# Performance work log

Hardware: AMD Instinct MI355X
Metric: run time of the kernel (lower is better)

Reference implementation:

```python
import jax, jax.numpy as jnp
import numpy as np

N_NODES = 100000
N_EDGES = 1600000
N_GRAPHS = 512
NODE_DIM = 64   # len(node_indices)
GRAPH_DIM = 16  # len(graph_indices) == graph_channels
HIDDEN = 128
OUT = 8


def setup_inputs() -> dict:
    key = jax.random.key(0)
    ks = jax.random.split(key, 12)
    x = jax.random.normal(ks[0], (N_NODES, NODE_DIM + GRAPH_DIM), dtype=jnp.float32)
    edge_index = jax.random.randint(ks[1], (2, N_EDGES), 0, N_NODES, dtype=jnp.int64)
    batch = jnp.sort(jax.random.randint(ks[2], (N_NODES,), 0, N_GRAPHS, dtype=jnp.int64))
    def lin(k, fan_in, fan_out):
        lim = 1.0 / np.sqrt(fan_in)
        return jax.random.uniform(k, (fan_in, fan_out), jnp.float32, -lim, lim)
    return {
        "x": x, "edge_index": edge_index, "batch": batch,
        "W1": lin(ks[3], NODE_DIM, HIDDEN), "b1": jnp.zeros((HIDDEN,), jnp.float32),
        "W2": lin(ks[4], HIDDEN, HIDDEN),   "b2": jnp.zeros((HIDDEN,), jnp.float32),
        "Wm1": lin(ks[5], HIDDEN + GRAPH_DIM, HIDDEN), "bm1": jnp.zeros((HIDDEN,), jnp.float32),
        "Wm2": lin(ks[6], HIDDEN, OUT), "bm2": jnp.zeros((OUT,), jnp.float32),
    }


def _gcn_conv(h_in, src, dst, W, b):
    # PyG GCNConv: h = X W; out = D^{-1/2}(A+I)D^{-1/2} h + b, deg over A+I.
    h = h_in @ W                                        # [N, H]
    deg = jnp.zeros((N_NODES,), h.dtype).at[dst].add(1.0) + 1.0  # +1 self loop
    dinv = jax.lax.rsqrt(deg)                           # [N]
    norm = dinv[src] * dinv[dst]                        # [E]
    out = jnp.zeros_like(h).at[dst].add(norm[:, None] * h[src])
    out = out + (dinv * dinv)[:, None] * h              # self-loop term
    return out + b


def _mean_pool(v, batch):
    cnt = jax.ops.segment_sum(jnp.ones((v.shape[0],), v.dtype), batch, num_segments=N_GRAPHS)
    s = jax.ops.segment_sum(v, batch, num_segments=N_GRAPHS)
    return s / jnp.maximum(cnt, 1.0)[:, None]


def reference(x, edge_index, batch, W1, b1, W2, b2, Wm1, bm1, Wm2, bm2):
    src, dst = edge_index[0], edge_index[1]
    node_t = x[:, :NODE_DIM]                 # node_indices slice
    graph_t = _mean_pool(x[:, NODE_DIM:], batch)  # graph_indices slice, pooled [G, 16]
    h = _gcn_conv(node_t, src, dst, W1, b1)
    h = jax.nn.relu(h)                       # dropout is identity in eval mode
    h = _gcn_conv(h, src, dst, W2, b2)
    g = _mean_pool(h, batch)                 # [G, H]
    g = jnp.concatenate([g, graph_t], axis=1)
    g = jax.nn.relu(g @ Wm1 + bm1)
    return g @ Wm2 + bm2                     # [G, OUT]
```

## Files before the change

### kernel.cpp

```cpp
#include <hip/hip_runtime.h>
#include <hip/hip_bf16.h>

#define N_NODES 100000
#define N_EDGES 1600000
#define N_GRAPHS 512
#define NODE_DIM 64
#define GRAPH_DIM 16
#define HIDDEN 128
#define OUT_DIM 8

#define NBUCKETS 391
#define BIN_CAP 8192
#define EPB 4096

__device__ __forceinline__ float bflo(unsigned u) { return __uint_as_float(u << 16); }
__device__ __forceinline__ float bfhi(unsigned u) { return __uint_as_float(u & 0xffff0000u); }


__global__ __launch_bounds__(256) void k_binplace(const int* __restrict__ src,
                                                  const int* __restrict__ dst,
                                                  int* __restrict__ gcur,
                                                  unsigned* __restrict__ bin) {
    __shared__ int cnt[NBUCKETS];
    __shared__ int base[NBUCKETS];
    int t = threadIdx.x;
    for (int i = t; i < NBUCKETS; i += 256) cnt[i] = 0;
    __syncthreads();
    int e0 = blockIdx.x * EPB;
#pragma unroll
    for (int k = 0; k < EPB / 256; k++) {
        int e = e0 + k * 256 + t;
        if (e < N_EDGES) atomicAdd(&cnt[dst[e] >> 8], 1);
    }
    __syncthreads();
    for (int i = t; i < NBUCKETS; i += 256) {
        int c = cnt[i];
        base[i] = (c > 0) ? atomicAdd(&gcur[i], c) : 0;
        cnt[i] = 0;
    }
    __syncthreads();
#pragma unroll
    for (int k = 0; k < EPB / 256; k++) {
        int e = e0 + k * 256 + t;
        if (e < N_EDGES) {
            int d = dst[e];
            int b = d >> 8;
            int p = atomicAdd(&cnt[b], 1);
            bin[(size_t)b * BIN_CAP + base[b] + p] = ((unsigned)src[e] << 8) | (unsigned)(d & 255);
        }
    }
}


__global__ __launch_bounds__(256) void k_build(const int* __restrict__ gcur,
                                               const unsigned* __restrict__ bin,
                                               float* __restrict__ dinv,
                                               int2* __restrict__ rowse,
                                               int* __restrict__ csr,
                                               float* __restrict__ gt_sum) {
    __shared__ int cnt[256];
    __shared__ int sc[256];
    __shared__ int rsl[256];
    int b = blockIdx.x, t = threadIdx.x;
    if (b < 32) gt_sum[b * 256 + t] = 0.0f;
    cnt[t] = 0;
    __syncthreads();
    int n = gcur[b];
    const unsigned* seg = bin + (size_t)b * BIN_CAP;
    for (int i = t; i < n; i += 256) atomicAdd(&cnt[seg[i] & 255u], 1);
    __syncthreads();
    int deg = cnt[t];
    sc[t] = deg;
    __syncthreads();
    for (int o = 1; o < 256; o <<= 1) {
        int u = (t >= o) ? sc[t - o] : 0;
        __syncthreads();
        sc[t] += u;
        __syncthreads();
    }
    int rs = b * BIN_CAP + sc[t] - deg;
    int node = b * 256 + t;
    if (node < N_NODES) {
        dinv[node] = rsqrtf((float)deg + 1.0f);
        rowse[node] = make_int2(rs, rs + deg);
    }
    rsl[t] = rs;
    cnt[t] = 0;
    __syncthreads();
    for (int i = t; i < n; i += 256) {
        unsigned e = seg[i];
        int dlidx = (int)(e & 255u);
        csr[rsl[dlidx] + atomicAdd(&cnt[dlidx], 1)] = (int)(e >> 8);
    }
}


__global__ __launch_bounds__(256) void k_packstat(const float* __restrict__ x,
                                                  const int* __restrict__ batch,
                                                  ushort* __restrict__ xb,
                                                  float* __restrict__ gt_sum) {
    int t = threadIdx.x;
    int i0 = blockIdx.x * 64;
    for (int idx = t; idx < 64 * 32; idx += 256) {
        int node = i0 + (idx >> 5);
        if (node < N_NODES) {
            int c2 = idx & 31;
            float2 v = *(const float2*)&x[(size_t)node * 80 + c2 * 2];
            __hip_bfloat16 lo = __float2bfloat16(v.x);
            __hip_bfloat16 hi = __float2bfloat16(v.y);
            ushort2 pv = make_ushort2(*(ushort*)&lo, *(ushort*)&hi);
            ((ushort2*)xb)[(size_t)node * 32 + c2] = pv;
        }
    }
    int c = t & 15, sub = t >> 4;
    int iend = min(i0 + 64, N_NODES);
    float acc = 0.0f;
    int g = -1;
    for (int i = i0 + sub; i < iend; i += 16) {
        int bi = batch[i];
        if (bi != g) {
            if (g >= 0) atomicAdd(&gt_sum[g * GRAPH_DIM + c], acc);
            acc = 0.0f; g = bi;
        }
        acc += x[(size_t)i * 80 + NODE_DIM + c];
    }
    if (g >= 0) atomicAdd(&gt_sum[g * GRAPH_DIM + c], acc);
}


#define LDX(s_) __uint_as_float((unsigned)xb[(size_t)(s_)*64 + lane] << 16)

__global__ __launch_bounds__(256) void k_conv1(const int* __restrict__ csr,
                                               const int2* __restrict__ rowse,
                                               const float* __restrict__ dinv,
                                               const ushort* __restrict__ xb,
                                               const float* __restrict__ W,
                                               const float* __restrict__ bias,
                                               ushort* __restrict__ C,
                                               float* __restrict__ gsum2) {
    __shared__ float zs[8][64];
    int t = threadIdx.x;
    if (blockIdx.x < 256) gsum2[blockIdx.x * 256 + t] = 0.0f;
    int w = t >> 6, lane = t & 63;
    int nA = blockIdx.x * 8 + w * 2;
    int nB = nA + 1;
    int2 seA = rowse[nA];
    int2 seB = rowse[nB];
    int kA = seA.x, reA = seA.y;
    int kB = seB.x, reB = seB.y;
    float dA = dinv[nA], dB = dinv[nB];
    float aA0 = 0.f, aA1 = 0.f, aA2 = 0.f, aA3 = 0.f;
    float aB0 = 0.f, aB1 = 0.f, aB2 = 0.f, aB3 = 0.f;
    while (kA + 4 <= reA && kB + 4 <= reB) {
        int a0 = csr[kA], a1 = csr[kA + 1], a2 = csr[kA + 2], a3 = csr[kA + 3];
        int b0 = csr[kB], b1 = csr[kB + 1], b2 = csr[kB + 2], b3 = csr[kB + 3];
        float wa0 = dinv[a0] * dA, wa1 = dinv[a1] * dA, wa2 = dinv[a2] * dA, wa3 = dinv[a3] * dA;
        float wb0 = dinv[b0] * dB, wb1 = dinv[b1] * dB, wb2 = dinv[b2] * dB, wb3 = dinv[b3] * dB;
        float vA0 = LDX(a0), vA1 = LDX(a1), vA2 = LDX(a2), vA3 = LDX(a3);
        float vB0 = LDX(b0), vB1 = LDX(b1), vB2 = LDX(b2), vB3 = LDX(b3);
        aA0 += wa0 * vA0; aA1 += wa1 * vA1; aA2 += wa2 * vA2; aA3 += wa3 * vA3;
        aB0 += wb0 * vB0; aB1 += wb1 * vB1; aB2 += wb2 * vB2; aB3 += wb3 * vB3;
        kA += 4; kB += 4;
    }
    while (kA + 4 <= reA) {
        int a0 = csr[kA], a1 = csr[kA + 1], a2 = csr[kA + 2], a3 = csr[kA + 3];
        float wa0 = dinv[a0] * dA, wa1 = dinv[a1] * dA, wa2 = dinv[a2] * dA, wa3 = dinv[a3] * dA;
        float v0 = LDX(a0), v1 = LDX(a1), v2 = LDX(a2), v3 = LDX(a3);
        aA0 += wa0 * v0; aA1 += wa1 * v1; aA2 += wa2 * v2; aA3 += wa3 * v3;
        kA += 4;
    }
    while (kB + 4 <= reB) {
        int b0 = csr[kB], b1 = csr[kB + 1], b2 = csr[kB + 2], b3 = csr[kB + 3];
        float wb0 = dinv[b0] * dB, wb1 = dinv[b1] * dB, wb2 = dinv[b2] * dB, wb3 = dinv[b3] * dB;
        float v0 = LDX(b0), v1 = LDX(b1), v2 = LDX(b2), v3 = LDX(b3);
        aB0 += wb0 * v0; aB1 += wb1 * v1; aB2 += wb2 * v2; aB3 += wb3 * v3;
        kB += 4;
    }
    while (kA < reA && kB < reB) {
        int a0 = csr[kA]; int b0 = csr[kB];
        aA0 += dinv[a0] * dA * LDX(a0);
        aB0 += dinv[b0] * dB * LDX(b0);
        kA++; kB++;
    }
    while (kA < reA) { int a0 = csr[kA]; aA0 += dinv[a0] * dA * LDX(a0); kA++; }
    while (kB < reB) { int b0 = csr[kB]; aB0 += dinv[b0] * dB * LDX(b0); kB++; }
    zs[w * 2][lane]     = aA0 + aA1 + aA2 + aA3 + dA * dA * LDX(nA);
    zs[w * 2 + 1][lane] = aB0 + aB1 + aB2 + aB3 + dB * dB * LDX(nB);
    __syncthreads();
    {
        int j = t & 127;
        int hf = t >> 7;
        float acc[4];
#pragma unroll
        for (int m = 0; m < 4; m++) acc[m] = 0.0f;
        for (int k = 0; k < 64; k++) {
            float wk = W[k * 128 + j];
#pragma unroll
            for (int m = 0; m < 4; m++) acc[m] += zs[hf * 4 + m][k] * wk;
        }
        float b = bias[j];
        size_t row0 = (size_t)blockIdx.x * 8 + hf * 4;
#pragma unroll
        for (int m = 0; m < 4; m++) {
            float v = fmaxf(acc[m] + b, 0.0f);
            __hip_bfloat16 hv = __float2bfloat16(v);
            C[(row0 + m) * 128 + j] = *(ushort*)&hv;
        }
    }
}


__global__ __launch_bounds__(256) void k_gather2(const int* __restrict__ csr,
                                                 const int2* __restrict__ rowse,
                                                 const float* __restrict__ dinv,
                                                 const unsigned* __restrict__ h,
                                                 const int* __restrict__ batch,
                                                 float* __restrict__ gsum2) {
    __shared__ float2 red[8][64];
    int w = threadIdx.x >> 6, lane = threadIdx.x & 63;
    int nA = blockIdx.x * 8 + w * 2;
    int nB = nA + 1;
    int2 seA = rowse[nA];
    int2 seB = rowse[nB];
    int kA = seA.x, reA = seA.y;
    int kB = seB.x, reB = seB.y;
    float dA = dinv[nA], dB = dinv[nB];
    float2 aA0 = {0.f,0.f}, aA1 = {0.f,0.f}, aA2 = {0.f,0.f}, aA3 = {0.f,0.f};
    float2 aB0 = {0.f,0.f}, aB1 = {0.f,0.f}, aB2 = {0.f,0.f}, aB3 = {0.f,0.f};
#define FMA2(acc_, w_, u_) { acc_.x += (w_) * bflo(u_); acc_.y += (w_) * bfhi(u_); }
    while (kA + 4 <= reA && kB + 4 <= reB) {
        int a0 = csr[kA], a1 = csr[kA + 1], a2 = csr[kA + 2], a3 = csr[kA + 3];
        int b0 = csr[kB], b1 = csr[kB + 1], b2 = csr[kB + 2], b3 = csr[kB + 3];
        float wa0 = dinv[a0] * dA, wa1 = dinv[a1] * dA, wa2 = dinv[a2] * dA, wa3 = dinv[a3] * dA;
        float wb0 = dinv[b0] * dB, wb1 = dinv[b1] * dB, wb2 = dinv[b2] * dB, wb3 = dinv[b3] * dB;
        unsigned uA0 = h[(size_t)a0 * 64 + lane], uA1 = h[(size_t)a1 * 64 + lane];
        unsigned uA2 = h[(size_t)a2 * 64 + lane], uA3 = h[(size_t)a3 * 64 + lane];
        unsigned uB0 = h[(size_t)b0 * 64 + lane], uB1 = h[(size_t)b1 * 64 + lane];
        unsigned uB2 = h[(size_t)b2 * 64 + lane], uB3 = h[(size_t)b3 * 64 + lane];
        FMA2(aA0, wa0, uA0); FMA2(aA1, wa1, uA1); FMA2(aA2, wa2, uA2); FMA2(aA3, wa3, uA3);
        FMA2(aB0, wb0, uB0); FMA2(aB1, wb1, uB1); FMA2(aB2, wb2, uB2); FMA2(aB3, wb3, uB3);
        kA += 4; kB += 4;
    }
    while (kA + 4 <= reA) {
        int a0 = csr[kA], a1 = csr[kA + 1], a2 = csr[kA + 2], a3 = csr[kA + 3];
        float wa0 = dinv[a0] * dA, wa1 = dinv[a1] * dA, wa2 = dinv[a2] * dA, wa3 = dinv[a3] * dA;
        unsigned u0 = h[(size_t)a0 * 64 + lane], u1 = h[(size_t)a1 * 64 + lane];
        unsigned u2 = h[(size_t)a2 * 64 + lane], u3 = h[(size_t)a3 * 64 + lane];
        FMA2(aA0, wa0, u0); FMA2(aA1, wa1, u1); FMA2(aA2, wa2, u2); FMA2(aA3, wa3, u3);
        kA += 4;
    }
    while (kB + 4 <= reB) {
        int b0 = csr[kB], b1 = csr[kB + 1], b2 = csr[kB + 2], b3 = csr[kB + 3];
        float wb0 = dinv[b0] * dB, wb1 = dinv[b1] * dB, wb2 = dinv[b2] * dB, wb3 = dinv[b3] * dB;
        unsigned u0 = h[(size_t)b0 * 64 + lane], u1 = h[(size_t)b1 * 64 + lane];
        unsigned u2 = h[(size_t)b2 * 64 + lane], u3 = h[(size_t)b3 * 64 + lane];
        FMA2(aB0, wb0, u0); FMA2(aB1, wb1, u1); FMA2(aB2, wb2, u2); FMA2(aB3, wb3, u3);
        kB += 4;
    }
    while (kA < reA && kB < reB) {
        int a0 = csr[kA]; int b0 = csr[kB];
        float wa0 = dinv[a0] * dA, wb0 = dinv[b0] * dB;
        unsigned uA = h[(size_t)a0 * 64 + lane], uB = h[(size_t)b0 * 64 + lane];
        FMA2(aA0, wa0, uA); FMA2(aB0, wb0, uB);
        kA++; kB++;
    }
    while (kA < reA) {
        int a0 = csr[kA];
        unsigned u = h[(size_t)a0 * 64 + lane];
        FMA2(aA0, dinv[a0] * dA, u); kA++;
    }
    while (kB < reB) {
        int b0 = csr[kB];
        unsigned u = h[(size_t)b0 * 64 + lane];
        FMA2(aB0, dinv[b0] * dB, u); kB++;
    }
#undef FMA2
    unsigned usA = h[(size_t)nA * 64 + lane];
    unsigned usB = h[(size_t)nB * 64 + lane];
    float2 rA, rB;
    rA.x = aA0.x + aA1.x + aA2.x + aA3.x + dA * dA * bflo(usA);
    rA.y = aA0.y + aA1.y + aA2.y + aA3.y + dA * dA * bfhi(usA);
    rB.x = aB0.x + aB1.x + aB2.x + aB3.x + dB * dB * bflo(usB);
    rB.y = aB0.y + aB1.y + aB2.y + aB3.y + dB * dB * bfhi(usB);
    red[w * 2][lane] = rA;
    red[w * 2 + 1][lane] = rB;
    __syncthreads();
    int g0 = batch[blockIdx.x * 8];
    int g7 = batch[blockIdx.x * 8 + 7];
    if (g0 == g7) {
        if (w == 0) {
            float sx = 0.f, sy = 0.f;
#pragma unroll
            for (int q = 0; q < 8; q++) { sx += red[q][lane].x; sy += red[q][lane].y; }
            atomicAdd(&gsum2[g0 * 128 + 2 * lane], sx);
            atomicAdd(&gsum2[g0 * 128 + 2 * lane + 1], sy);
        }
    } else {
        int gA = batch[nA], gB = batch[nB];
        atomicAdd(&gsum2[gA * 128 + 2 * lane], rA.x);
        atomicAdd(&gsum2[gA * 128 + 2 * lane + 1], rA.y);
        atomicAdd(&gsum2[gB * 128 + 2 * lane], rB.x);
        atomicAdd(&gsum2[gB * 128 + 2 * lane + 1], rB.y);
    }
}


__global__ __launch_bounds__(128) void k_mlp(const float* __restrict__ gsum2,
                                             const float* __restrict__ gt_sum,
                                             const int* __restrict__ batch,
                                             const float* __restrict__ W2,
                                             const float* __restrict__ b2,
                                             const float* __restrict__ Wm1,
                                             const float* __restrict__ bm1,
                                             const float* __restrict__ Wm2,
                                             const float* __restrict__ bm2,
                                             float* __restrict__ out) {
    __shared__ float srow[HIDDEN];
    __shared__ float g144[HIDDEN + GRAPH_DIM];
    __shared__ float sm[HIDDEN];
    __shared__ int cnt_sh;
    int b = blockIdx.x;
    int j = threadIdx.x;
    float raw = gsum2[b * 128 + j];
    float gtraw = (j < GRAPH_DIM) ? gt_sum[b * GRAPH_DIM + j] : 0.0f;
    if (j == 0) {
        int lo = 0, hi = N_NODES;
        while (lo < hi) { int m = (lo + hi) >> 1; if (batch[m] < b) lo = m + 1; else hi = m; }
        int a = lo;
        lo = 0; hi = N_NODES;
        while (lo < hi) { int m = (lo + hi) >> 1; if (batch[m] < b + 1) lo = m + 1; else hi = m; }
        cnt_sh = lo - a;
    }
    __syncthreads();
    float inv = 1.0f / fmaxf((float)cnt_sh, 1.0f);
    srow[j] = raw * inv;
    if (j < GRAPH_DIM) g144[128 + j] = gtraw * inv;
    __syncthreads();
    float z = b2[j];
    for (int k = 0; k < 128; k++) z += srow[k] * W2[k * 128 + j];
    g144[j] = z;
    __syncthreads();
    float acc = bm1[j];
    for (int k = 0; k < HIDDEN + GRAPH_DIM; k++) acc += g144[k] * Wm1[k * 128 + j];
    sm[j] = fmaxf(acc, 0.0f);
    __syncthreads();
    if (j < OUT_DIM) {
        float o = bm2[j];
        for (int k = 0; k < 128; k++) o += sm[k] * Wm2[k * OUT_DIM + j];
        out[b * OUT_DIM + j] = o;
    }
}

extern "C" void kernel_launch(void* const* d_in, const int* in_sizes, int n_in,
                              void* d_out, int out_size, void* d_ws, size_t ws_size,
                              hipStream_t stream) {
    const float* x    = (const float*)d_in[0];
    const int*   edge = (const int*)d_in[1];
    const int*   src  = edge;
    const int*   dst  = edge + N_EDGES;
    const int*   batch= (const int*)d_in[2];
    const float* W1   = (const float*)d_in[3];
    const float* b1   = (const float*)d_in[4];
    const float* W2   = (const float*)d_in[5];
    const float* b2   = (const float*)d_in[6];
    const float* Wm1  = (const float*)d_in[7];
    const float* bm1  = (const float*)d_in[8];
    const float* Wm2  = (const float*)d_in[9];
    const float* bm2  = (const float*)d_in[10];
    float* out = (float*)d_out;

    char* ws = (char*)d_ws;
    char* p = ws;
    unsigned* bin   = (unsigned*)p;  p += (size_t)NBUCKETS * BIN_CAP * 4;
    int*   csr      = (int*)p;       p += (size_t)NBUCKETS * BIN_CAP * 4;
    ushort* h1b     = (ushort*)p;    p += (size_t)N_NODES * 128 * 2;
    ushort* xb      = (ushort*)p;    p += (size_t)N_NODES * 64 * 2;
    int2*  rowse    = (int2*)p;      p += (size_t)N_NODES * 8;
    float* dinv     = (float*)p;     p += (size_t)N_NODES * 4;
    int*   gcur     = (int*)p;       p += (size_t)NBUCKETS * 4;
    float* gt_sum   = (float*)p;     p += (size_t)N_GRAPHS * GRAPH_DIM * 4;
    float* gsum2    = (float*)p;     p += (size_t)N_GRAPHS * 128 * 4;

    hipMemsetAsync(gcur, 0, (size_t)NBUCKETS * 4, stream);

    k_binplace<<<(N_EDGES + EPB - 1) / EPB, 256, 0, stream>>>(src, dst, gcur, bin);
    k_build<<<NBUCKETS, 256, 0, stream>>>(gcur, bin, dinv, rowse, csr, gt_sum);

    k_packstat<<<(N_NODES + 63) / 64, 256, 0, stream>>>(x, batch, xb, gt_sum);

    k_conv1<<<N_NODES / 8, 256, 0, stream>>>(csr, rowse, dinv, xb, W1, b1, h1b, gsum2);

    k_gather2<<<N_NODES / 8, 256, 0, stream>>>(csr, rowse, dinv,
                                               (const unsigned*)h1b, batch, gsum2);

    k_mlp<<<N_GRAPHS, 128, 0, stream>>>(gsum2, gt_sum, batch, W2, b2, Wm1, bm1, Wm2, bm2, out);
}
```

Measured before the change: 237.7 us.

## Fuse edge binning with feature packing and unroll gathers to 8 edges

Merges the edge-binning kernel and the x-to-bf16 pack / graph-feature pooling kernel into one launch with block-range dispatch. The gt_sum zeroing moves into the existing memset, which now also covers the adjacent gt_sum buffer. The gather loops in both conv kernels are unrolled to 8 edges per step to keep more loads in flight. This removes a launch and lets the two independent preprocessing phases overlap, at the cost of higher register pressure from the wider unroll.

```diff
diff --git a/kernel.cpp b/kernel.cpp
--- a/kernel.cpp
+++ b/kernel.cpp
@@ -12,42 +12,76 @@
 #define NBUCKETS 391
 #define BIN_CAP 8192
 #define EPB 4096
+#define NB_BIN 391
+#define NB_PACK 1563
 
 __device__ __forceinline__ float bflo(unsigned u) { return __uint_as_float(u << 16); }
 __device__ __forceinline__ float bfhi(unsigned u) { return __uint_as_float(u & 0xffff0000u); }
 
 
-__global__ __launch_bounds__(256) void k_binplace(const int* __restrict__ src,
-                                                  const int* __restrict__ dst,
-                                                  int* __restrict__ gcur,
-                                                  unsigned* __restrict__ bin) {
-    __shared__ int cnt[NBUCKETS];
-    __shared__ int base[NBUCKETS];
+__global__ __launch_bounds__(256) void k_binpack(const int* __restrict__ src,
+                                                 const int* __restrict__ dst,
+                                                 int* __restrict__ gcur,
+                                                 unsigned* __restrict__ bin,
+                                                 const float* __restrict__ x,
+                                                 const int* __restrict__ batch,
+                                                 ushort* __restrict__ xb,
+                                                 float* __restrict__ gt_sum) {
     int t = threadIdx.x;
-    for (int i = t; i < NBUCKETS; i += 256) cnt[i] = 0;
-    __syncthreads();
-    int e0 = blockIdx.x * EPB;
-#pragma unroll
-    for (int k = 0; k < EPB / 256; k++) {
-        int e = e0 + k * 256 + t;
-        if (e < N_EDGES) atomicAdd(&cnt[dst[e] >> 8], 1);
-    }
-    __syncthreads();
-    for (int i = t; i < NBUCKETS; i += 256) {
-        int c = cnt[i];
-        base[i] = (c > 0) ? atomicAdd(&gcur[i], c) : 0;
-        cnt[i] = 0;
-    }
-    __syncthreads();
-#pragma unroll
-    for (int k = 0; k < EPB / 256; k++) {
-        int e = e0 + k * 256 + t;
-        if (e < N_EDGES) {
-            int d = dst[e];
-            int b = d >> 8;
-            int p = atomicAdd(&cnt[b], 1);
-            bin[(size_t)b * BIN_CAP + base[b] + p] = ((unsigned)src[e] << 8) | (unsigned)(d & 255);
-        }
+    if (blockIdx.x < NB_BIN) {
+        __shared__ int cnt[NBUCKETS];
+        __shared__ int base[NBUCKETS];
+        for (int i = t; i < NBUCKETS; i += 256) cnt[i] = 0;
+        __syncthreads();
+        int e0 = blockIdx.x * EPB;
+#pragma unroll
+        for (int k = 0; k < EPB / 256; k++) {
+            int e = e0 + k * 256 + t;
+            if (e < N_EDGES) atomicAdd(&cnt[dst[e] >> 8], 1);
+        }
+        __syncthreads();
+        for (int i = t; i < NBUCKETS; i += 256) {
+            int c = cnt[i];
+            base[i] = (c > 0) ? atomicAdd(&gcur[i], c) : 0;
+            cnt[i] = 0;
+        }
+        __syncthreads();
+#pragma unroll
+        for (int k = 0; k < EPB / 256; k++) {
+            int e = e0 + k * 256 + t;
+            if (e < N_EDGES) {
+                int d = dst[e];
+                int b = d >> 8;
+                int p = atomicAdd(&cnt[b], 1);
+                bin[(size_t)b * BIN_CAP + base[b] + p] = ((unsigned)src[e] << 8) | (unsigned)(d & 255);
+            }
+        }
+    } else {
+        int i0 = (blockIdx.x - NB_BIN) * 64;
+        for (int idx = t; idx < 64 * 32; idx += 256) {
+            int node = i0 + (idx >> 5);
+            if (node < N_NODES) {
+                int c2 = idx & 31;
+                float2 v = *(const float2*)&x[(size_t)node * 80 + c2 * 2];
+                __hip_bfloat16 lo = __float2bfloat16(v.x);
+                __hip_bfloat16 hi = __float2bfloat16(v.y);
+                ushort2 pv = make_ushort2(*(ushort*)&lo, *(ushort*)&hi);
+                ((ushort2*)xb)[(size_t)node * 32 + c2] = pv;
+            }
+        }
+        int c = t & 15, sub = t >> 4;
+        int iend = min(i0 + 64, N_NODES);
+        float acc = 0.0f;
+        int g = -1;
+        for (int i = i0 + sub; i < iend; i += 16) {
+            int bi = batch[i];
+            if (bi != g) {
+                if (g >= 0) atomicAdd(&gt_sum[g * GRAPH_DIM + c], acc);
+                acc = 0.0f; g = bi;
+            }
+            acc += x[(size_t)i * 80 + NODE_DIM + c];
+        }
+        if (g >= 0) atomicAdd(&gt_sum[g * GRAPH_DIM + c], acc);
     }
 }
 
@@ -56,13 +90,11 @@
                                                const unsigned* __restrict__ bin,
                                                float* __restrict__ dinv,
                                                int2* __restrict__ rowse,
-                                               int* __restrict__ csr,
-                                               float* __restrict__ gt_sum) {
+                                               int* __restrict__ csr) {
     __shared__ int cnt[256];
     __shared__ int sc[256];
     __shared__ int rsl[256];
     int b = blockIdx.x, t = threadIdx.x;
-    if (b < 32) gt_sum[b * 256 + t] = 0.0f;
     cnt[t] = 0;
     __syncthreads();
     int n = gcur[b];
@@ -95,40 +127,27 @@
 }
 
 
-__global__ __launch_bounds__(256) void k_packstat(const float* __restrict__ x,
-                                                  const int* __restrict__ batch,
-                                                  ushort* __restrict__ xb,
-                                                  float* __restrict__ gt_sum) {
-    int t = threadIdx.x;
-    int i0 = blockIdx.x * 64;
-    for (int idx = t; idx < 64 * 32; idx += 256) {
-        int node = i0 + (idx >> 5);
-        if (node < N_NODES) {
-            int c2 = idx & 31;
-            float2 v = *(const float2*)&x[(size_t)node * 80 + c2 * 2];
-            __hip_bfloat16 lo = __float2bfloat16(v.x);
-            __hip_bfloat16 hi = __float2bfloat16(v.y);
-            ushort2 pv = make_ushort2(*(ushort*)&lo, *(ushort*)&hi);
-            ((ushort2*)xb)[(size_t)node * 32 + c2] = pv;
-        }
-    }
-    int c = t & 15, sub = t >> 4;
-    int iend = min(i0 + 64, N_NODES);
-    float acc = 0.0f;
-    int g = -1;
-    for (int i = i0 + sub; i < iend; i += 16) {
-        int bi = batch[i];
-        if (bi != g) {
-            if (g >= 0) atomicAdd(&gt_sum[g * GRAPH_DIM + c], acc);
-            acc = 0.0f; g = bi;
-        }
-        acc += x[(size_t)i * 80 + NODE_DIM + c];
-    }
-    if (g >= 0) atomicAdd(&gt_sum[g * GRAPH_DIM + c], acc);
-}
-
-
 #define LDX(s_) __uint_as_float((unsigned)xb[(size_t)(s_)*64 + lane] << 16)
+
+#define C1_E8(kX, dX, aX0, aX1, aX2, aX3) {                                          \
+    int s0 = csr[kX],     s1 = csr[kX + 1], s2 = csr[kX + 2], s3 = csr[kX + 3];      \
+    int s4 = csr[kX + 4], s5 = csr[kX + 5], s6 = csr[kX + 6], s7 = csr[kX + 7];      \
+    float w0 = dinv[s0] * dX, w1 = dinv[s1] * dX, w2 = dinv[s2] * dX, w3 = dinv[s3] * dX; \
+    float w4 = dinv[s4] * dX, w5 = dinv[s5] * dX, w6 = dinv[s6] * dX, w7 = dinv[s7] * dX; \
+    float v0 = LDX(s0), v1 = LDX(s1), v2 = LDX(s2), v3 = LDX(s3);                    \
+    float v4 = LDX(s4), v5 = LDX(s5), v6 = LDX(s6), v7 = LDX(s7);                    \
+    aX0 += w0 * v0; aX1 += w1 * v1; aX2 += w2 * v2; aX3 += w3 * v3;                  \
+    aX0 += w4 * v4; aX1 += w5 * v5; aX2 += w6 * v6; aX3 += w7 * v7; }
+
+#define C1_E4(kX, dX, aX0, aX1, aX2, aX3) {                                          \
+    int s0 = csr[kX], s1 = csr[kX + 1], s2 = csr[kX + 2], s3 = csr[kX + 3];          \
+    float w0 = dinv[s0] * dX, w1 = dinv[s1] * dX, w2 = dinv[s2] * dX, w3 = dinv[s3] * dX; \
+    float v0 = LDX(s0), v1 = LDX(s1), v2 = LDX(s2), v3 = LDX(s3);                    \
+    aX0 += w0 * v0; aX1 += w1 * v1; aX2 += w2 * v2; aX3 += w3 * v3; }
+
+#define C1_E1(kX, dX, aX0) {                                                         \
+    int s0 = csr[kX];                                                                \
+    aX0 += dinv[s0] * dX * LDX(s0); }
 
 __global__ __launch_bounds__(256) void k_conv1(const int* __restrict__ csr,
                                                const int2* __restrict__ rowse,
@@ -151,39 +170,23 @@
     float dA = dinv[nA], dB = dinv[nB];
     float aA0 = 0.f, aA1 = 0.f, aA2 = 0.f, aA3 = 0.f;
     float aB0 = 0.f, aB1 = 0.f, aB2 = 0.f, aB3 = 0.f;
+    while (kA + 8 <= reA && kB + 8 <= reB) {
+        C1_E8(kA, dA, aA0, aA1, aA2, aA3)
+        C1_E8(kB, dB, aB0, aB1, aB2, aB3)
+        kA += 8; kB += 8;
+    }
+    while (kA + 8 <= reA) { C1_E8(kA, dA, aA0, aA1, aA2, aA3) kA += 8; }
+    while (kB + 8 <= reB) { C1_E8(kB, dB, aB0, aB1, aB2, aB3) kB += 8; }
     while (kA + 4 <= reA && kB + 4 <= reB) {
-        int a0 = csr[kA], a1 = csr[kA + 1], a2 = csr[kA + 2], a3 = csr[kA + 3];
-        int b0 = csr[kB], b1 = csr[kB + 1], b2 = csr[kB + 2], b3 = csr[kB + 3];
-        float wa0 = dinv[a0] * dA, wa1 = dinv[a1] * dA, wa2 = dinv[a2] * dA, wa3 = dinv[a3] * dA;
-        float wb0 = dinv[b0] * dB, wb1 = dinv[b1] * dB, wb2 = dinv[b2] * dB, wb3 = dinv[b3] * dB;
-        float vA0 = LDX(a0), vA1 = LDX(a1), vA2 = LDX(a2), vA3 = LDX(a3);
-        float vB0 = LDX(b0), vB1 = LDX(b1), vB2 = LDX(b2), vB3 = LDX(b3);
-        aA0 += wa0 * vA0; aA1 += wa1 * vA1; aA2 += wa2 * vA2; aA3 += wa3 * vA3;
-        aB0 += wb0 * vB0; aB1 += wb1 * vB1; aB2 += wb2 * vB2; aB3 += wb3 * vB3;
+        C1_E4(kA, dA, aA0, aA1, aA2, aA3)
+        C1_E4(kB, dB, aB0, aB1, aB2, aB3)
         kA += 4; kB += 4;
     }
-    while (kA + 4 <= reA) {
-        int a0 = csr[kA], a1 = csr[kA + 1], a2 = csr[kA + 2], a3 = csr[kA + 3];
-        float wa0 = dinv[a0] * dA, wa1 = dinv[a1] * dA, wa2 = dinv[a2] * dA, wa3 = dinv[a3] * dA;
-        float v0 = LDX(a0), v1 = LDX(a1), v2 = LDX(a2), v3 = LDX(a3);
-        aA0 += wa0 * v0; aA1 += wa1 * v1; aA2 += wa2 * v2; aA3 += wa3 * v3;
-        kA += 4;
-    }
-    while (kB + 4 <= reB) {
-        int b0 = csr[kB], b1 = csr[kB + 1], b2 = csr[kB + 2], b3 = csr[kB + 3];
-        float wb0 = dinv[b0] * dB, wb1 = dinv[b1] * dB, wb2 = dinv[b2] * dB, wb3 = dinv[b3] * dB;
-        float v0 = LDX(b0), v1 = LDX(b1), v2 = LDX(b2), v3 = LDX(b3);
-        aB0 += wb0 * v0; aB1 += wb1 * v1; aB2 += wb2 * v2; aB3 += wb3 * v3;
-        kB += 4;
-    }
-    while (kA < reA && kB < reB) {
-        int a0 = csr[kA]; int b0 = csr[kB];
-        aA0 += dinv[a0] * dA * LDX(a0);
-        aB0 += dinv[b0] * dB * LDX(b0);
-        kA++; kB++;
-    }
-    while (kA < reA) { int a0 = csr[kA]; aA0 += dinv[a0] * dA * LDX(a0); kA++; }
-    while (kB < reB) { int b0 = csr[kB]; aB0 += dinv[b0] * dB * LDX(b0); kB++; }
+    while (kA + 4 <= reA) { C1_E4(kA, dA, aA0, aA1, aA2, aA3) kA += 4; }
+    while (kB + 4 <= reB) { C1_E4(kB, dB, aB0, aB1, aB2, aB3) kB += 4; }
+    while (kA < reA && kB < reB) { C1_E1(kA, dA, aA0) C1_E1(kB, dB, aB0) kA++; kB++; }
+    while (kA < reA) { C1_E1(kA, dA, aA0) kA++; }
+    while (kB < reB) { C1_E1(kB, dB, aB0) kB++; }
     zs[w * 2][lane]     = aA0 + aA1 + aA2 + aA3 + dA * dA * LDX(nA);
     zs[w * 2 + 1][lane] = aB0 + aB1 + aB2 + aB3 + dB * dB * LDX(nB);
     __syncthreads();
@@ -209,6 +212,32 @@
     }
 }
 
+
+#define FMA2(acc_, w_, u_) { acc_.x += (w_) * bflo(u_); acc_.y += (w_) * bfhi(u_); }
+
+#define G2_E8(kX, dX, aX0, aX1, aX2, aX3) {                                          \
+    int s0 = csr[kX],     s1 = csr[kX + 1], s2 = csr[kX + 2], s3 = csr[kX + 3];      \
+    int s4 = csr[kX + 4], s5 = csr[kX + 5], s6 = csr[kX + 6], s7 = csr[kX + 7];      \
+    float w0 = dinv[s0] * dX, w1 = dinv[s1] * dX, w2 = dinv[s2] * dX, w3 = dinv[s3] * dX; \
+    float w4 = dinv[s4] * dX, w5 = dinv[s5] * dX, w6 = dinv[s6] * dX, w7 = dinv[s7] * dX; \
+    unsigned u0 = h[(size_t)s0 * 64 + lane], u1 = h[(size_t)s1 * 64 + lane];         \
+    unsigned u2 = h[(size_t)s2 * 64 + lane], u3 = h[(size_t)s3 * 64 + lane];         \
+    unsigned u4 = h[(size_t)s4 * 64 + lane], u5 = h[(size_t)s5 * 64 + lane];         \
+    unsigned u6 = h[(size_t)s6 * 64 + lane], u7 = h[(size_t)s7 * 64 + lane];         \
+    FMA2(aX0, w0, u0) FMA2(aX1, w1, u1) FMA2(aX2, w2, u2) FMA2(aX3, w3, u3)          \
+    FMA2(aX0, w4, u4) FMA2(aX1, w5, u5) FMA2(aX2, w6, u6) FMA2(aX3, w7, u7) }
+
+#define G2_E4(kX, dX, aX0, aX1, aX2, aX3) {                                          \
+    int s0 = csr[kX], s1 = csr[kX + 1], s2 = csr[kX + 2], s3 = csr[kX + 3];          \
+    float w0 = dinv[s0] * dX, w1 = dinv[s1] * dX, w2 = dinv[s2] * dX, w3 = dinv[s3] * dX; \
+    unsigned u0 = h[(size_t)s0 * 64 + lane], u1 = h[(size_t)s1 * 64 + lane];         \
+    unsigned u2 = h[(size_t)s2 * 64 + lane], u3 = h[(size_t)s3 * 64 + lane];         \
+    FMA2(aX0, w0, u0) FMA2(aX1, w1, u1) FMA2(aX2, w2, u2) FMA2(aX3, w3, u3) }
+
+#define G2_E1(kX, dX, aX0) {                                                         \
+    int s0 = csr[kX];                                                                \
+    unsigned u0 = h[(size_t)s0 * 64 + lane];                                         \
+    FMA2(aX0, dinv[s0] * dX, u0) }
 
 __global__ __launch_bounds__(256) void k_gather2(const int* __restrict__ csr,
                                                  const int2* __restrict__ rowse,
@@ -227,54 +256,23 @@
     float dA = dinv[nA], dB = dinv[nB];
     float2 aA0 = {0.f,0.f}, aA1 = {0.f,0.f}, aA2 = {0.f,0.f}, aA3 = {0.f,0.f};
     float2 aB0 = {0.f,0.f}, aB1 = {0.f,0.f}, aB2 = {0.f,0.f}, aB3 = {0.f,0.f};
-#define FMA2(acc_, w_, u_) { acc_.x += (w_) * bflo(u_); acc_.y += (w_) * bfhi(u_); }
+    while (kA + 8 <= reA && kB + 8 <= reB) {
+        G2_E8(kA, dA, aA0, aA1, aA2, aA3)
+        G2_E8(kB, dB, aB0, aB1, aB2, aB3)
+        kA += 8; kB += 8;
+    }
+    while (kA + 8 <= reA) { G2_E8(kA, dA, aA0, aA1, aA2, aA3) kA += 8; }
+    while (kB + 8 <= reB) { G2_E8(kB, dB, aB0, aB1, aB2, aB3) kB += 8; }
     while (kA + 4 <= reA && kB + 4 <= reB) {
-        int a0 = csr[kA], a1 = csr[kA + 1], a2 = csr[kA + 2], a3 = csr[kA + 3];
-        int b0 = csr[kB], b1 = csr[kB + 1], b2 = csr[kB + 2], b3 = csr[kB + 3];
-        float wa0 = dinv[a0] * dA, wa1 = dinv[a1] * dA, wa2 = dinv[a2] * dA, wa3 = dinv[a3] * dA;
-        float wb0 = dinv[b0] * dB, wb1 = dinv[b1] * dB, wb2 = dinv[b2] * dB, wb3 = dinv[b3] * dB;
-        unsigned uA0 = h[(size_t)a0 * 64 + lane], uA1 = h[(size_t)a1 * 64 + lane];
-        unsigned uA2 = h[(size_t)a2 * 64 + lane], uA3 = h[(size_t)a3 * 64 + lane];
-        unsigned uB0 = h[(size_t)b0 * 64 + lane], uB1 = h[(size_t)b1 * 64 + lane];
-        unsigned uB2 = h[(size_t)b2 * 64 + lane], uB3 = h[(size_t)b3 * 64 + lane];
-        FMA2(aA0, wa0, uA0); FMA2(aA1, wa1, uA1); FMA2(aA2, wa2, uA2); FMA2(aA3, wa3, uA3);
-        FMA2(aB0, wb0, uB0); FMA2(aB1, wb1, uB1); FMA2(aB2, wb2, uB2); FMA2(aB3, wb3, uB3);
+        G2_E4(kA, dA, aA0, aA1, aA2, aA3)
+        G2_E4(kB, dB, aB0, aB1, aB2, aB3)
         kA += 4; kB += 4;
     }
-    while (kA + 4 <= reA) {
-        int a0 = csr[kA], a1 = csr[kA + 1], a2 = csr[kA + 2], a3 = csr[kA + 3];
-        float wa0 = dinv[a0] * dA, wa1 = dinv[a1] * dA, wa2 = dinv[a2] * dA, wa3 = dinv[a3] * dA;
-        unsigned u0 = h[(size_t)a0 * 64 + lane], u1 = h[(size_t)a1 * 64 + lane];
-        unsigned u2 = h[(size_t)a2 * 64 + lane], u3 = h[(size_t)a3 * 64 + lane];
-        FMA2(aA0, wa0, u0); FMA2(aA1, wa1, u1); FMA2(aA2, wa2, u2); FMA2(aA3, wa3, u3);
-        kA += 4;
-    }
-    while (kB + 4 <= reB) {
-        int b0 = csr[kB], b1 = csr[kB + 1], b2 = csr[kB + 2], b3 = csr[kB + 3];
-        float wb0 = dinv[b0] * dB, wb1 = dinv[b1] * dB, wb2 = dinv[b2] * dB, wb3 = dinv[b3] * dB;
-        unsigned u0 = h[(size_t)b0 * 64 + lane], u1 = h[(size_t)b1 * 64 + lane];
-        unsigned u2 = h[(size_t)b2 * 64 + lane], u3 = h[(size_t)b3 * 64 + lane];
-        FMA2(aB0, wb0, u0); FMA2(aB1, wb1, u1); FMA2(aB2, wb2, u2); FMA2(aB3, wb3, u3);
-        kB += 4;
-    }
-    while (kA < reA && kB < reB) {
-        int a0 = csr[kA]; int b0 = csr[kB];
-        float wa0 = dinv[a0] * dA, wb0 = dinv[b0] * dB;
-        unsigned uA = h[(size_t)a0 * 64 + lane], uB = h[(size_t)b0 * 64 + lane];
-        FMA2(aA0, wa0, uA); FMA2(aB0, wb0, uB);
-        kA++; kB++;
-    }
-    while (kA < reA) {
-        int a0 = csr[kA];
-        unsigned u = h[(size_t)a0 * 64 + lane];
-        FMA2(aA0, dinv[a0] * dA, u); kA++;
-    }
-    while (kB < reB) {
-        int b0 = csr[kB];
-        unsigned u = h[(size_t)b0 * 64 + lane];
-        FMA2(aB0, dinv[b0] * dB, u); kB++;
-    }
-#undef FMA2
+    while (kA + 4 <= reA) { G2_E4(kA, dA, aA0, aA1, aA2, aA3) kA += 4; }
+    while (kB + 4 <= reB) { G2_E4(kB, dB, aB0, aB1, aB2, aB3) kB += 4; }
+    while (kA < reA && kB < reB) { G2_E1(kA, dA, aA0) G2_E1(kB, dB, aB0) kA++; kB++; }
+    while (kA < reA) { G2_E1(kA, dA, aA0) kA++; }
+    while (kB < reB) { G2_E1(kB, dB, aB0) kB++; }
     unsigned usA = h[(size_t)nA * 64 + lane];
     unsigned usB = h[(size_t)nB * 64 + lane];
     float2 rA, rB;
@@ -381,12 +379,11 @@
     float* gt_sum   = (float*)p;     p += (size_t)N_GRAPHS * GRAPH_DIM * 4;
     float* gsum2    = (float*)p;     p += (size_t)N_GRAPHS * 128 * 4;
 
-    hipMemsetAsync(gcur, 0, (size_t)NBUCKETS * 4, stream);
-
-    k_binplace<<<(N_EDGES + EPB - 1) / EPB, 256, 0, stream>>>(src, dst, gcur, bin);
-    k_build<<<NBUCKETS, 256, 0, stream>>>(gcur, bin, dinv, rowse, csr, gt_sum);
-
-    k_packstat<<<(N_NODES + 63) / 64, 256, 0, stream>>>(x, batch, xb, gt_sum);
+    hipMemsetAsync(gcur, 0, (size_t)NBUCKETS * 4 + (size_t)N_GRAPHS * GRAPH_DIM * 4, stream);
+
+    k_binpack<<<NB_BIN + NB_PACK, 256, 0, stream>>>(src, dst, gcur, bin, x, batch, xb, gt_sum);
+
+    k_build<<<NBUCKETS, 256, 0, stream>>>(gcur, bin, dinv, rowse, csr);
 
     k_conv1<<<N_NODES / 8, 256, 0, stream>>>(csr, rowse, dinv, xb, W1, b1, h1b, gsum2);
 
```

New measurement: 236.2 us. No clear change (-0.7%).
